# Kernel optimization log

Measured on AMD Instinct MI355X. Metric: run time of the kernel, lower is better.

## Reference

```python
import jax, jax.numpy as jnp
import numpy as np

D_MODEL = 512
N_HEADS = 8
D_K = D_MODEL // N_HEADS


def setup_inputs() -> dict:
    key = jax.random.key(0)
    ks = jax.random.split(key, 11)
    B, S = 4, 2048
    scale = 1.0 / np.sqrt(D_MODEL)
    inp = {
        'q': jax.random.normal(ks[0], (B, S, D_MODEL), jnp.float32),
        'k': jax.random.normal(ks[1], (B, S, D_MODEL), jnp.float32),
        'v': jax.random.normal(ks[2], (B, S, D_MODEL), jnp.float32),
        'wq': jax.random.normal(ks[3], (D_MODEL, D_MODEL), jnp.float32) * scale,
        'wk': jax.random.normal(ks[4], (D_MODEL, D_MODEL), jnp.float32) * scale,
        'wv': jax.random.normal(ks[5], (D_MODEL, D_MODEL), jnp.float32) * scale,
        'wo': jax.random.normal(ks[6], (D_MODEL, D_MODEL), jnp.float32) * scale,
        'bq': jax.random.normal(ks[7], (D_MODEL,), jnp.float32) * 0.01,
        'bk': jax.random.normal(ks[8], (D_MODEL,), jnp.float32) * 0.01,
        'bv': jax.random.normal(ks[9], (D_MODEL,), jnp.float32) * 0.01,
        'bo': jax.random.normal(ks[10], (D_MODEL,), jnp.float32) * 0.01,
    }
    return inp


def reference(q, k, v, wq, wk, wv, wo, bq, bk, bv, bo):
    b, s, d = q.shape
    # projections; torch Linear is x @ W.T + b
    qh = (q @ wq.T + bq).reshape(b, s, N_HEADS, D_K).transpose(0, 2, 1, 3)  # [b,h,s,dk]
    kh = (k @ wk.T + bk).reshape(b, s, N_HEADS, D_K).transpose(0, 2, 1, 3)
    vh = (v @ wv.T + bv).reshape(b, s, N_HEADS, D_K).transpose(0, 2, 1, 3)
    att = jnp.einsum('bhqd,bhkd->bhqk', qh, kh) / jnp.sqrt(jnp.float32(D_K))
    att = jax.nn.softmax(att, axis=-1)
    out = jnp.einsum('bhqk,bhkd->bhqd', att, vh)  # [b,h,s,dk]
    out = out.transpose(0, 2, 1, 3).reshape(b, s, d)
    return out @ wo.T + bo
```

## Files before the change

kernel.cpp:

```cpp
#include <hip/hip_runtime.h>

#define D_MODEL 512
#define NH 8
#define DK 64
#define SEQ 2048
#define NB 4

typedef __bf16 bf16x8 __attribute__((ext_vector_type(8)));
typedef float floatx4 __attribute__((ext_vector_type(4)));
typedef float floatx16 __attribute__((ext_vector_type(16)));

typedef __attribute__((address_space(1))) const unsigned int glb_u32;
typedef __attribute__((address_space(3))) unsigned int lds_u32;

__device__ __forceinline__ void gload_lds16(const unsigned short* g, unsigned short* l) {
    __builtin_amdgcn_global_load_lds((glb_u32*)g, (lds_u32*)l, 16, 0, 0);
}

__device__ inline unsigned int pack2bf(float lo, float hi) {
    unsigned int a = __float_as_uint(lo) + 0x8000u;
    unsigned int b = __float_as_uint(hi) + 0x8000u;
    return __builtin_amdgcn_perm(b, a, 0x07060302u);
}
__device__ inline unsigned short f2bf(float f) {
    return (unsigned short)((__float_as_uint(f) + 0x8000u) >> 16);
}
__device__ inline unsigned int scale2bf(unsigned int u, float s) {
    float lo = __uint_as_float(u << 16) * s;
    float hi = __uint_as_float(u & 0xFFFF0000u) * s;
    return pack2bf(lo, hi);
}

__global__ __launch_bounds__(256) void convert_kernel(
    const float* __restrict__ q, const float* __restrict__ k, const float* __restrict__ v,
    const float* __restrict__ wq, const float* __restrict__ wk, const float* __restrict__ wv,
    const float* __restrict__ wo, unsigned short* __restrict__ Xbf,
    unsigned short* __restrict__ Wbf)
{
    const int bid = blockIdx.x;
    const float* src;
    unsigned short* dst;
    size_t off;
    if (bid < 6144) {
        const int which = bid >> 11;
        src = (which == 0) ? q : (which == 1) ? k : v;
        dst = Xbf + (size_t)which * 4194304;
        off = ((size_t)(bid & 2047) * 256 + threadIdx.x) * 8;
    } else {
        const int wb = bid - 6144;
        const int which = wb >> 7;
        src = (which == 0) ? wq : (which == 1) ? wk : (which == 2) ? wv : wo;
        dst = Wbf + (size_t)which * 262144;
        off = ((size_t)(wb & 127) * 256 + threadIdx.x) * 8;
    }
    float4 a = *(const float4*)(src + off);
    float4 b = *(const float4*)(src + off + 4);
    uint4 r;
    r.x = pack2bf(a.x, a.y); r.y = pack2bf(a.z, a.w);
    r.z = pack2bf(b.x, b.y); r.w = pack2bf(b.z, b.w);
    *(uint4*)(dst + off) = r;
}

__global__ __launch_bounds__(256) void proj_qkv_kernel(
    const unsigned short* __restrict__ Xbf, const unsigned short* __restrict__ Wbf,
    const float* __restrict__ bq, const float* __restrict__ bk, const float* __restrict__ bv,
    unsigned short* __restrict__ Qh, unsigned short* __restrict__ Kh,
    unsigned short* __restrict__ VhT)
{
    const int which = blockIdx.z;
    const unsigned short* A = Xbf + (size_t)which * 4194304;
    const unsigned short* B = Wbf + (size_t)which * 262144;
    const float* bias = (which == 0) ? bq : (which == 1) ? bk : bv;

    const int n0 = blockIdx.x * 128;
    const int m0 = blockIdx.y * 128;

    __shared__ unsigned short lds[17408];

    const int tid  = threadIdx.x;
    const int lane = tid & 63;
    const int wid  = tid >> 6;
    const int quad = lane >> 4;
    const int l16  = lane & 15;
    const int wr   = (wid >> 1) * 64;
    const int wc   = (wid & 1) * 64;

    const int srow8 = lane >> 3;
    const int scg   = (lane & 7) ^ (srow8 & 7);

    floatx4 acc[4][4];
#pragma unroll
    for (int i = 0; i < 4; ++i)
#pragma unroll
        for (int j = 0; j < 4; ++j) acc[i][j] = {0.f, 0.f, 0.f, 0.f};

    for (int kt = 0; kt < 8; ++kt) {
        const int kk0 = kt * 64;
        __syncthreads();
#pragma unroll
        for (int t = 0; t < 4; ++t) {
            const int i = wid * 4 + t;
            const int row = i * 8 + srow8;
            gload_lds16(A + (size_t)(m0 + row) * 512 + kk0 + scg * 8, &lds[i * 512]);
            gload_lds16(B + (size_t)(n0 + row) * 512 + kk0 + scg * 8, &lds[8192 + i * 512]);
        }
        __syncthreads();

        bf16x8 af[4][2], bf[4][2];
#pragma unroll
        for (int kk = 0; kk < 2; ++kk) {
            const int c = kk * 4 + quad;
#pragma unroll
            for (int mi = 0; mi < 4; ++mi) {
                const int rA = wr + mi * 16 + l16;
                af[mi][kk] = *(const bf16x8*)(&lds[rA * 64 + ((c ^ (rA & 7)) * 8)]);
            }
#pragma unroll
            for (int ni = 0; ni < 4; ++ni) {
                const int rB = wc + ni * 16 + l16;
                bf[ni][kk] = *(const bf16x8*)(&lds[8192 + rB * 64 + ((c ^ (rB & 7)) * 8)]);
            }
        }
#pragma unroll
        for (int kk = 0; kk < 2; ++kk)
#pragma unroll
            for (int mi = 0; mi < 4; ++mi)
#pragma unroll
                for (int ni = 0; ni < 4; ++ni)
                    acc[mi][ni] = __builtin_amdgcn_mfma_f32_16x16x32_bf16(
                        af[mi][kk], bf[ni][kk], acc[mi][ni], 0, 0, 0);
    }

    float bs[4];
#pragma unroll
    for (int ni = 0; ni < 4; ++ni) bs[ni] = bias[n0 + wc + ni * 16 + l16];

    __syncthreads();
#pragma unroll
    for (int mi = 0; mi < 4; ++mi)
#pragma unroll
        for (int ni = 0; ni < 4; ++ni)
#pragma unroll
            for (int r = 0; r < 4; ++r)
                lds[(wr + mi * 16 + quad * 4 + r) * 136 + wc + ni * 16 + l16] =
                    f2bf(acc[mi][ni][r] + bs[ni]);
    __syncthreads();

    const int b = m0 >> 11;
    if (which != 2) {
        unsigned short* dst = (which == 0) ? Qh : Kh;
#pragma unroll
        for (int j = 0; j < 8; ++j) {
            const int chunk = j * 256 + tid;
            const int srow  = chunk >> 4;
            const int col   = (chunk & 15) * 8;
            const int h  = (n0 + col) >> 6;
            const int dk = col & 63;
            const int s  = (m0 & 2047) + srow;
            uint4 vv = *(const uint4*)(&lds[srow * 136 + col]);
            *(uint4*)(dst + ((size_t)(b * NH + h) * SEQ + s) * DK + dk) = vv;
        }
    } else {
#pragma unroll
        for (int j = 0; j < 8; ++j) {
            const int chunk = j * 256 + tid;
            const int d    = chunk >> 4;
            const int sc8  = (chunk & 15) * 8;
            const int h  = (n0 + d) >> 6;
            const int dk = (n0 + d) & 63;
            unsigned short tmp[8];
#pragma unroll
            for (int i = 0; i < 8; ++i) tmp[i] = lds[(sc8 + i) * 136 + d];
            const size_t s0 = (size_t)(m0 & 2047) + sc8;
            *(uint4*)(VhT + ((size_t)(b * NH + h) * DK + dk) * SEQ + s0) = *(const uint4*)tmp;
        }
    }
}

__global__ __launch_bounds__(256, 2) void flash_kernel(
    const unsigned short* __restrict__ Qh, const unsigned short* __restrict__ Kh,
    const unsigned short* __restrict__ VhT, unsigned short* __restrict__ AO)
{
    const int qt = blockIdx.x, h = blockIdx.y, b = blockIdx.z;
    const size_t bh = (size_t)b * NH + h;
    const unsigned short* Qp = Qh + bh * SEQ * DK;
    const unsigned short* Kp = Kh + bh * SEQ * DK;
    const unsigned short* Vp = VhT + bh * DK * SEQ;

    __shared__ unsigned short smem[17920];

    const int tid  = threadIdx.x;
    const int lane = tid & 63;
    const int wid  = tid >> 6;
    const int g    = wid >> 1;
    const int ws   = wid & 1;
    const int hh   = lane >> 5;
    const int l32  = lane & 31;

    const int srow = lane >> 3;
    const int schk = (lane & 7) ^ srow;

    const float SC = 0.18033688f;
    bf16x8 qf[4][2];
#pragma unroll
    for (int nt = 0; nt < 2; ++nt) {
        const int qrow = qt * 128 + ws * 64 + nt * 32 + l32;
#pragma unroll
        for (int ks = 0; ks < 4; ++ks) {
            uint4 u = *(const uint4*)(Qp + (size_t)qrow * 64 + ks * 16 + hh * 8);
            union { uint4 u4; bf16x8 v; } w;
            w.u4.x = scale2bf(u.x, SC); w.u4.y = scale2bf(u.y, SC);
            w.u4.z = scale2bf(u.z, SC); w.u4.w = scale2bf(u.w, SC);
            qf[ks][nt] = w.v;
        }
    }

    floatx16 oacc[2][2];
#pragma unroll
    for (int i = 0; i < 2; ++i)
#pragma unroll
        for (int j = 0; j < 2; ++j)
#pragma unroll
            for (int r = 0; r < 16; ++r) oacc[i][j][r] = 0.f;
    float lsA[2] = {0.f, 0.f}, lsB[2] = {0.f, 0.f};

    for (int kt = 0; kt < 16; ++kt) {
        __syncthreads();
#pragma unroll
        for (int t = 0; t < 8; ++t) {
            const int id = wid * 8 + t;
            const int gg = id >> 4;
            const int kv = (id >> 3) & 1;
            const int j  = id & 7;
            const int row = j * 8 + srow;
            const int sk0 = (gg * 16 + kt) * 64;
            if (kv == 0)
                gload_lds16(Kp + (size_t)(sk0 + row) * 64 + schk * 8,
                            &smem[gg * 8192 + j * 512]);
            else
                gload_lds16(Vp + (size_t)row * 2048 + sk0 + schk * 8,
                            &smem[gg * 8192 + 4096 + j * 512]);
        }
        __syncthreads();

        const unsigned short* Kb = &smem[g * 8192];
        const unsigned short* Vb = &smem[g * 8192 + 4096];

        floatx16 sc[2][2];
#pragma unroll
        for (int i = 0; i < 2; ++i)
#pragma unroll
            for (int j = 0; j < 2; ++j)
#pragma unroll
                for (int r = 0; r < 16; ++r) sc[i][j][r] = 0.f;
#pragma unroll
        for (int ks = 0; ks < 4; ++ks) {
            const int c = ks * 2 + hh;
            bf16x8 kf[2];
#pragma unroll
            for (int mt = 0; mt < 2; ++mt) {
                const int row = mt * 32 + l32;
                kf[mt] = *(const bf16x8*)(&Kb[row * 64 + ((c ^ (row & 7)) * 8)]);
            }
#pragma unroll
            for (int mt = 0; mt < 2; ++mt)
#pragma unroll
                for (int nt = 0; nt < 2; ++nt)
                    sc[mt][nt] = __builtin_amdgcn_mfma_f32_32x32x16_bf16(
                        kf[mt], qf[ks][nt], sc[mt][nt], 0, 0, 0);
        }

#pragma unroll
        for (int st = 0; st < 2; ++st)
#pragma unroll
            for (int nt = 0; nt < 2; ++nt)
#pragma unroll
                for (int r = 0; r < 16; ++r) {
                    float p = __builtin_amdgcn_exp2f(sc[st][nt][r]);
                    sc[st][nt][r] = p;
                    if (r & 1) lsB[nt] += p; else lsA[nt] += p;
                }

        bf16x8 vf[2][4];
#pragma unroll
        for (int ksp = 0; ksp < 4; ++ksp) {
            const int c = ksp * 2 + hh;
#pragma unroll
            for (int vt = 0; vt < 2; ++vt) {
                const int row = vt * 32 + l32;
                vf[vt][ksp] = *(const bf16x8*)(&Vb[row * 64 + ((c ^ (row & 7)) * 8)]);
            }
        }

#pragma unroll
        for (int st = 0; st < 2; ++st)
#pragma unroll
            for (int nt = 0; nt < 2; ++nt) {
                int p[8];
#pragma unroll
                for (int i = 0; i < 8; ++i)
                    p[i] = (int)pack2bf(sc[st][nt][2 * i], sc[st][nt][2 * i + 1]);
                const int e0 = __shfl_xor(hh ? p[0] : p[2], 32, 64);
                const int e1 = __shfl_xor(hh ? p[1] : p[3], 32, 64);
                const int e2 = __shfl_xor(hh ? p[4] : p[6], 32, 64);
                const int e3 = __shfl_xor(hh ? p[5] : p[7], 32, 64);
                union { int i4[4]; bf16x8 v; } b0, b1;
                b0.i4[0] = hh ? e0 : p[0];
                b0.i4[1] = hh ? e1 : p[1];
                b0.i4[2] = hh ? p[2] : e0;
                b0.i4[3] = hh ? p[3] : e1;
                b1.i4[0] = hh ? e2 : p[4];
                b1.i4[1] = hh ? e3 : p[5];
                b1.i4[2] = hh ? p[6] : e2;
                b1.i4[3] = hh ? p[7] : e3;
                const int k0 = st * 2;
#pragma unroll
                for (int vt = 0; vt < 2; ++vt) {
                    oacc[vt][nt] = __builtin_amdgcn_mfma_f32_32x32x16_bf16(
                        vf[vt][k0], b0.v, oacc[vt][nt], 0, 0, 0);
                    oacc[vt][nt] = __builtin_amdgcn_mfma_f32_32x32x16_bf16(
                        vf[vt][k0 + 1], b1.v, oacc[vt][nt], 0, 0, 0);
                }
            }
    }

    __syncthreads();
    float* pf = (float*)smem;
    float* lf = (float*)(&smem[17408]);
    if (g == 1) {
#pragma unroll
        for (int vt = 0; vt < 2; ++vt)
#pragma unroll
            for (int nt = 0; nt < 2; ++nt) {
                const int base = ws * 4352 + lane * 68 + (vt * 2 + nt) * 16;
#pragma unroll
                for (int r4 = 0; r4 < 4; ++r4) {
                    floatx4 t = {oacc[vt][nt][r4 * 4 + 0], oacc[vt][nt][r4 * 4 + 1],
                                 oacc[vt][nt][r4 * 4 + 2], oacc[vt][nt][r4 * 4 + 3]};
                    *(floatx4*)(&pf[base + r4 * 4]) = t;
                }
            }
        lf[ws * 128 + 0 * 64 + lane] = lsA[0] + lsB[0];
        lf[ws * 128 + 1 * 64 + lane] = lsA[1] + lsB[1];
    }
    __syncthreads();
    float linv[2];
    if (g == 0) {
#pragma unroll
        for (int nt = 0; nt < 2; ++nt) {
            float lm = lsA[nt] + lsB[nt] + lf[ws * 128 + nt * 64 + lane];
            lm += __shfl_xor(lm, 32, 64);
            linv[nt] = 1.0f / lm;
        }
#pragma unroll
        for (int vt = 0; vt < 2; ++vt)
#pragma unroll
            for (int nt = 0; nt < 2; ++nt) {
                const int base = ws * 4352 + lane * 68 + (vt * 2 + nt) * 16;
#pragma unroll
                for (int r4 = 0; r4 < 4; ++r4) {
                    floatx4 t = *(const floatx4*)(&pf[base + r4 * 4]);
#pragma unroll
                    for (int e = 0; e < 4; ++e)
                        oacc[vt][nt][r4 * 4 + e] =
                            (oacc[vt][nt][r4 * 4 + e] + t[e]) * linv[nt];
                }
            }
    }
    __syncthreads();
    if (g == 0) {
#pragma unroll
        for (int vt = 0; vt < 2; ++vt)
#pragma unroll
            for (int nt = 0; nt < 2; ++nt) {
                const int qrow = ws * 64 + nt * 32 + l32;
#pragma unroll
                for (int i = 0; i < 8; ++i) {
                    const int dko = vt * 32 + 8 * (i >> 1) + 2 * (i & 1) + 4 * hh;
                    *(unsigned int*)(&smem[qrow * 72 + dko]) =
                        pack2bf(oacc[vt][nt][2 * i], oacc[vt][nt][2 * i + 1]);
                }
            }
    }
    __syncthreads();
#pragma unroll
    for (int i = 0; i < 4; ++i) {
        const int idx = i * 256 + tid;
        const int row = idx >> 3;
        const int c   = idx & 7;
        *(uint4*)(AO + ((size_t)b * SEQ + qt * 128 + row) * 512 + h * 64 + c * 8) =
            *(const uint4*)(&smem[row * 72 + c * 8]);
    }
}

__global__ __launch_bounds__(256) void outproj_kernel(
    const unsigned short* __restrict__ AO, const unsigned short* __restrict__ Wbf,
    const float* __restrict__ bo, float* __restrict__ out)
{
    const unsigned short* B = Wbf + (size_t)3 * 262144;
    const int n0 = blockIdx.x * 128;
    const int m0 = blockIdx.y * 64;

    __shared__ unsigned short lds[12288];

    const int tid  = threadIdx.x;
    const int lane = tid & 63;
    const int wid  = tid >> 6;
    const int quad = lane >> 4;
    const int l16  = lane & 15;
    const int wr   = (wid >> 1) * 32;
    const int wc   = (wid & 1) * 64;

    const int srow8 = lane >> 3;
    const int scg   = (lane & 7) ^ (srow8 & 7);

    floatx4 acc[2][4];
#pragma unroll
    for (int i = 0; i < 2; ++i)
#pragma unroll
        for (int j = 0; j < 4; ++j) acc[i][j] = {0.f, 0.f, 0.f, 0.f};

    for (int kt = 0; kt < 8; ++kt) {
        const int kk0 = kt * 64;
        __syncthreads();
#pragma unroll
        for (int t = 0; t < 2; ++t) {
            const int i = wid * 2 + t;
            const int row = i * 8 + srow8;
            gload_lds16(AO + (size_t)(m0 + row) * 512 + kk0 + scg * 8, &lds[i * 512]);
        }
#pragma unroll
        for (int t = 0; t < 4; ++t) {
            const int i = wid * 4 + t;
            const int row = i * 8 + srow8;
            gload_lds16(B + (size_t)(n0 + row) * 512 + kk0 + scg * 8, &lds[4096 + i * 512]);
        }
        __syncthreads();

        bf16x8 af[2][2], bf[4][2];
#pragma unroll
        for (int kk = 0; kk < 2; ++kk) {
            const int c = kk * 4 + quad;
#pragma unroll
            for (int mi = 0; mi < 2; ++mi) {
                const int rA = wr + mi * 16 + l16;
                af[mi][kk] = *(const bf16x8*)(&lds[rA * 64 + ((c ^ (rA & 7)) * 8)]);
            }
#pragma unroll
            for (int ni = 0; ni < 4; ++ni) {
                const int rB = wc + ni * 16 + l16;
                bf[ni][kk] = *(const bf16x8*)(&lds[4096 + rB * 64 + ((c ^ (rB & 7)) * 8)]);
            }
        }
#pragma unroll
        for (int kk = 0; kk < 2; ++kk)
#pragma unroll
            for (int mi = 0; mi < 2; ++mi)
#pragma unroll
                for (int ni = 0; ni < 4; ++ni)
                    acc[mi][ni] = __builtin_amdgcn_mfma_f32_16x16x32_bf16(
                        af[mi][kk], bf[ni][kk], acc[mi][ni], 0, 0, 0);
    }

#pragma unroll
    for (int mi = 0; mi < 2; ++mi)
#pragma unroll
        for (int ni = 0; ni < 4; ++ni) {
            const int n = n0 + wc + ni * 16 + l16;
            const float bsv = bo[n];
#pragma unroll
            for (int r = 0; r < 4; ++r) {
                const int m = m0 + wr + mi * 16 + quad * 4 + r;
                out[(size_t)m * 512 + n] = acc[mi][ni][r] + bsv;
            }
        }
}

extern "C" void kernel_launch(void* const* d_in, const int* in_sizes, int n_in,
                              void* d_out, int out_size, void* d_ws, size_t ws_size,
                              hipStream_t stream) {
    const float* q  = (const float*)d_in[0];
    const float* k  = (const float*)d_in[1];
    const float* v  = (const float*)d_in[2];
    const float* wq = (const float*)d_in[3];
    const float* wk = (const float*)d_in[4];
    const float* wv = (const float*)d_in[5];
    const float* wo = (const float*)d_in[6];
    const float* bq = (const float*)d_in[7];
    const float* bk = (const float*)d_in[8];
    const float* bv = (const float*)d_in[9];
    const float* bo = (const float*)d_in[10];

    const size_t headElems = (size_t)NB * NH * SEQ * DK;
    unsigned short* Qh  = (unsigned short*)d_ws;
    unsigned short* Kh  = Qh + headElems;
    unsigned short* VhT = Kh + headElems;
    unsigned short* AO  = VhT + headElems;
    unsigned short* Xbf = AO + headElems;
    unsigned short* Wbf = Xbf + 3 * headElems;
    float* out = (float*)d_out;

    convert_kernel<<<dim3(6656), 256, 0, stream>>>(q, k, v, wq, wk, wv, wo, Xbf, Wbf);
    proj_qkv_kernel<<<dim3(4, 64, 3), 256, 0, stream>>>(
        Xbf, Wbf, bq, bk, bv, Qh, Kh, VhT);
    flash_kernel<<<dim3(SEQ / 128, NH, NB), 256, 0, stream>>>(Qh, Kh, VhT, AO);
    outproj_kernel<<<dim3(4, 128), 256, 0, stream>>>(AO, Wbf, bo, out);
}
```

Before: 192.5 us.

## Halve flash query tile to 64 rows and raise occupancy to 4 blocks per CU

The flash attention kernel now handles 64 query rows per block instead of 128, so each wave holds one 32-row Q fragment and half the score and output accumulators. Launch bounds go to 4 blocks per CU, shared memory shrinks, and V fragments are loaded from LDS just before each PV MFMA rather than all up front. The grid doubles to 1024 blocks. This cuts register pressure and raises occupancy to better hide latency, but each block reloads the full K/V for fewer queries, doubling K/V global and LDS traffic per unit of work.

Result: slower. 201.3 us (+4.6%).

```diff
diff --git a/kernel.cpp b/kernel.cpp
--- a/kernel.cpp
+++ b/kernel.cpp
@@ -177,7 +177,7 @@
     }
 }
 
-__global__ __launch_bounds__(256, 2) void flash_kernel(
+__global__ __launch_bounds__(256, 4) void flash_kernel(
     const unsigned short* __restrict__ Qh, const unsigned short* __restrict__ Kh,
     const unsigned short* __restrict__ VhT, unsigned short* __restrict__ AO)
 {
@@ -187,7 +187,7 @@
     const unsigned short* Kp = Kh + bh * SEQ * DK;
     const unsigned short* Vp = VhT + bh * DK * SEQ;
 
-    __shared__ unsigned short smem[17920];
+    __shared__ unsigned short smem[16384];
 
     const int tid  = threadIdx.x;
     const int lane = tid & 63;
@@ -201,28 +201,25 @@
     const int schk = (lane & 7) ^ srow;
 
     const float SC = 0.18033688f;
-    bf16x8 qf[4][2];
-#pragma unroll
-    for (int nt = 0; nt < 2; ++nt) {
-        const int qrow = qt * 128 + ws * 64 + nt * 32 + l32;
+    bf16x8 qf[4];
+    {
+        const int qrow = qt * 64 + ws * 32 + l32;
 #pragma unroll
         for (int ks = 0; ks < 4; ++ks) {
             uint4 u = *(const uint4*)(Qp + (size_t)qrow * 64 + ks * 16 + hh * 8);
             union { uint4 u4; bf16x8 v; } w;
             w.u4.x = scale2bf(u.x, SC); w.u4.y = scale2bf(u.y, SC);
             w.u4.z = scale2bf(u.z, SC); w.u4.w = scale2bf(u.w, SC);
-            qf[ks][nt] = w.v;
-        }
-    }
-
-    floatx16 oacc[2][2];
+            qf[ks] = w.v;
+        }
+    }
+
+    floatx16 oacc[2];
 #pragma unroll
     for (int i = 0; i < 2; ++i)
 #pragma unroll
-        for (int j = 0; j < 2; ++j)
-#pragma unroll
-            for (int r = 0; r < 16; ++r) oacc[i][j][r] = 0.f;
-    float lsA[2] = {0.f, 0.f}, lsB[2] = {0.f, 0.f};
+        for (int r = 0; r < 16; ++r) oacc[i][r] = 0.f;
+    float lsA = 0.f, lsB = 0.f;
 
     for (int kt = 0; kt < 16; ++kt) {
         __syncthreads();
@@ -246,149 +243,116 @@
         const unsigned short* Kb = &smem[g * 8192];
         const unsigned short* Vb = &smem[g * 8192 + 4096];
 
-        floatx16 sc[2][2];
+        floatx16 sc[2];
 #pragma unroll
         for (int i = 0; i < 2; ++i)
 #pragma unroll
-            for (int j = 0; j < 2; ++j)
-#pragma unroll
-                for (int r = 0; r < 16; ++r) sc[i][j][r] = 0.f;
+            for (int r = 0; r < 16; ++r) sc[i][r] = 0.f;
 #pragma unroll
         for (int ks = 0; ks < 4; ++ks) {
             const int c = ks * 2 + hh;
-            bf16x8 kf[2];
 #pragma unroll
             for (int mt = 0; mt < 2; ++mt) {
                 const int row = mt * 32 + l32;
-                kf[mt] = *(const bf16x8*)(&Kb[row * 64 + ((c ^ (row & 7)) * 8)]);
-            }
-#pragma unroll
-            for (int mt = 0; mt < 2; ++mt)
-#pragma unroll
-                for (int nt = 0; nt < 2; ++nt)
-                    sc[mt][nt] = __builtin_amdgcn_mfma_f32_32x32x16_bf16(
-                        kf[mt], qf[ks][nt], sc[mt][nt], 0, 0, 0);
+                bf16x8 kf = *(const bf16x8*)(&Kb[row * 64 + ((c ^ (row & 7)) * 8)]);
+                sc[mt] = __builtin_amdgcn_mfma_f32_32x32x16_bf16(
+                    kf, qf[ks], sc[mt], 0, 0, 0);
+            }
         }
 
 #pragma unroll
         for (int st = 0; st < 2; ++st)
 #pragma unroll
-            for (int nt = 0; nt < 2; ++nt)
-#pragma unroll
-                for (int r = 0; r < 16; ++r) {
-                    float p = __builtin_amdgcn_exp2f(sc[st][nt][r]);
-                    sc[st][nt][r] = p;
-                    if (r & 1) lsB[nt] += p; else lsA[nt] += p;
-                }
-
-        bf16x8 vf[2][4];
-#pragma unroll
-        for (int ksp = 0; ksp < 4; ++ksp) {
-            const int c = ksp * 2 + hh;
+            for (int r = 0; r < 16; ++r) {
+                float p = __builtin_amdgcn_exp2f(sc[st][r]);
+                sc[st][r] = p;
+                if (r & 1) lsB += p; else lsA += p;
+            }
+
+#pragma unroll
+        for (int st = 0; st < 2; ++st) {
+            int p[8];
+#pragma unroll
+            for (int i = 0; i < 8; ++i)
+                p[i] = (int)pack2bf(sc[st][2 * i], sc[st][2 * i + 1]);
+            const int e0 = __shfl_xor(hh ? p[0] : p[2], 32, 64);
+            const int e1 = __shfl_xor(hh ? p[1] : p[3], 32, 64);
+            const int e2 = __shfl_xor(hh ? p[4] : p[6], 32, 64);
+            const int e3 = __shfl_xor(hh ? p[5] : p[7], 32, 64);
+            union { int i4[4]; bf16x8 v; } b0, b1;
+            b0.i4[0] = hh ? e0 : p[0];
+            b0.i4[1] = hh ? e1 : p[1];
+            b0.i4[2] = hh ? p[2] : e0;
+            b0.i4[3] = hh ? p[3] : e1;
+            b1.i4[0] = hh ? e2 : p[4];
+            b1.i4[1] = hh ? e3 : p[5];
+            b1.i4[2] = hh ? p[6] : e2;
+            b1.i4[3] = hh ? p[7] : e3;
 #pragma unroll
             for (int vt = 0; vt < 2; ++vt) {
                 const int row = vt * 32 + l32;
-                vf[vt][ksp] = *(const bf16x8*)(&Vb[row * 64 + ((c ^ (row & 7)) * 8)]);
-            }
-        }
-
-#pragma unroll
-        for (int st = 0; st < 2; ++st)
-#pragma unroll
-            for (int nt = 0; nt < 2; ++nt) {
-                int p[8];
-#pragma unroll
-                for (int i = 0; i < 8; ++i)
-                    p[i] = (int)pack2bf(sc[st][nt][2 * i], sc[st][nt][2 * i + 1]);
-                const int e0 = __shfl_xor(hh ? p[0] : p[2], 32, 64);
-                const int e1 = __shfl_xor(hh ? p[1] : p[3], 32, 64);
-                const int e2 = __shfl_xor(hh ? p[4] : p[6], 32, 64);
-                const int e3 = __shfl_xor(hh ? p[5] : p[7], 32, 64);
-                union { int i4[4]; bf16x8 v; } b0, b1;
-                b0.i4[0] = hh ? e0 : p[0];
-                b0.i4[1] = hh ? e1 : p[1];
-                b0.i4[2] = hh ? p[2] : e0;
-                b0.i4[3] = hh ? p[3] : e1;
-                b1.i4[0] = hh ? e2 : p[4];
-                b1.i4[1] = hh ? e3 : p[5];
-                b1.i4[2] = hh ? p[6] : e2;
-                b1.i4[3] = hh ? p[7] : e3;
-                const int k0 = st * 2;
-#pragma unroll
-                for (int vt = 0; vt < 2; ++vt) {
-                    oacc[vt][nt] = __builtin_amdgcn_mfma_f32_32x32x16_bf16(
-                        vf[vt][k0], b0.v, oacc[vt][nt], 0, 0, 0);
-                    oacc[vt][nt] = __builtin_amdgcn_mfma_f32_32x32x16_bf16(
-                        vf[vt][k0 + 1], b1.v, oacc[vt][nt], 0, 0, 0);
-                }
-            }
+                const int c0 = (st * 2) * 2 + hh;
+                const int c1 = (st * 2 + 1) * 2 + hh;
+                bf16x8 vf0 = *(const bf16x8*)(&Vb[row * 64 + ((c0 ^ (row & 7)) * 8)]);
+                bf16x8 vf1 = *(const bf16x8*)(&Vb[row * 64 + ((c1 ^ (row & 7)) * 8)]);
+                oacc[vt] = __builtin_amdgcn_mfma_f32_32x32x16_bf16(
+                    vf0, b0.v, oacc[vt], 0, 0, 0);
+                oacc[vt] = __builtin_amdgcn_mfma_f32_32x32x16_bf16(
+                    vf1, b1.v, oacc[vt], 0, 0, 0);
+            }
+        }
     }
 
     __syncthreads();
     float* pf = (float*)smem;
-    float* lf = (float*)(&smem[17408]);
+    float* lf = (float*)(&smem[8704]);
     if (g == 1) {
+        const int base = (ws * 64 + lane) * 34;
 #pragma unroll
         for (int vt = 0; vt < 2; ++vt)
 #pragma unroll
-            for (int nt = 0; nt < 2; ++nt) {
-                const int base = ws * 4352 + lane * 68 + (vt * 2 + nt) * 16;
-#pragma unroll
-                for (int r4 = 0; r4 < 4; ++r4) {
-                    floatx4 t = {oacc[vt][nt][r4 * 4 + 0], oacc[vt][nt][r4 * 4 + 1],
-                                 oacc[vt][nt][r4 * 4 + 2], oacc[vt][nt][r4 * 4 + 3]};
-                    *(floatx4*)(&pf[base + r4 * 4]) = t;
-                }
-            }
-        lf[ws * 128 + 0 * 64 + lane] = lsA[0] + lsB[0];
-        lf[ws * 128 + 1 * 64 + lane] = lsA[1] + lsB[1];
-    }
-    __syncthreads();
-    float linv[2];
+            for (int r4 = 0; r4 < 4; ++r4) {
+                floatx4 t = {oacc[vt][r4 * 4 + 0], oacc[vt][r4 * 4 + 1],
+                             oacc[vt][r4 * 4 + 2], oacc[vt][r4 * 4 + 3]};
+                *(floatx4*)(&pf[base + vt * 16 + r4 * 4]) = t;
+            }
+        lf[ws * 64 + lane] = lsA + lsB;
+    }
+    __syncthreads();
     if (g == 0) {
-#pragma unroll
-        for (int nt = 0; nt < 2; ++nt) {
-            float lm = lsA[nt] + lsB[nt] + lf[ws * 128 + nt * 64 + lane];
-            lm += __shfl_xor(lm, 32, 64);
-            linv[nt] = 1.0f / lm;
-        }
+        float lm = lsA + lsB + lf[ws * 64 + lane];
+        lm += __shfl_xor(lm, 32, 64);
+        const float linv = 1.0f / lm;
+        const int base = (ws * 64 + lane) * 34;
 #pragma unroll
         for (int vt = 0; vt < 2; ++vt)
 #pragma unroll
-            for (int nt = 0; nt < 2; ++nt) {
-                const int base = ws * 4352 + lane * 68 + (vt * 2 + nt) * 16;
-#pragma unroll
-                for (int r4 = 0; r4 < 4; ++r4) {
-                    floatx4 t = *(const floatx4*)(&pf[base + r4 * 4]);
-#pragma unroll
-                    for (int e = 0; e < 4; ++e)
-                        oacc[vt][nt][r4 * 4 + e] =
-                            (oacc[vt][nt][r4 * 4 + e] + t[e]) * linv[nt];
-                }
+            for (int r4 = 0; r4 < 4; ++r4) {
+                floatx4 t = *(const floatx4*)(&pf[base + vt * 16 + r4 * 4]);
+#pragma unroll
+                for (int e = 0; e < 4; ++e)
+                    oacc[vt][r4 * 4 + e] = (oacc[vt][r4 * 4 + e] + t[e]) * linv;
             }
     }
     __syncthreads();
     if (g == 0) {
+        const int qrowl = ws * 32 + l32;
 #pragma unroll
         for (int vt = 0; vt < 2; ++vt)
 #pragma unroll
-            for (int nt = 0; nt < 2; ++nt) {
-                const int qrow = ws * 64 + nt * 32 + l32;
-#pragma unroll
-                for (int i = 0; i < 8; ++i) {
-                    const int dko = vt * 32 + 8 * (i >> 1) + 2 * (i & 1) + 4 * hh;
-                    *(unsigned int*)(&smem[qrow * 72 + dko]) =
-                        pack2bf(oacc[vt][nt][2 * i], oacc[vt][nt][2 * i + 1]);
-                }
-            }
-    }
-    __syncthreads();
-#pragma unroll
-    for (int i = 0; i < 4; ++i) {
+            for (int i = 0; i < 8; ++i) {
+                const int dko = vt * 32 + 8 * (i >> 1) + 2 * (i & 1) + 4 * hh;
+                *(unsigned int*)(&smem[qrowl * 72 + dko]) =
+                    pack2bf(oacc[vt][2 * i], oacc[vt][2 * i + 1]);
+            }
+    }
+    __syncthreads();
+#pragma unroll
+    for (int i = 0; i < 2; ++i) {
         const int idx = i * 256 + tid;
         const int row = idx >> 3;
         const int c   = idx & 7;
-        *(uint4*)(AO + ((size_t)b * SEQ + qt * 128 + row) * 512 + h * 64 + c * 8) =
+        *(uint4*)(AO + ((size_t)b * SEQ + qt * 64 + row) * 512 + h * 64 + c * 8) =
             *(const uint4*)(&smem[row * 72 + c * 8]);
     }
 }
@@ -503,6 +467,6 @@
     convert_kernel<<<dim3(6656), 256, 0, stream>>>(q, k, v, wq, wk, wv, wo, Xbf, Wbf);
     proj_qkv_kernel<<<dim3(4, 64, 3), 256, 0, stream>>>(
         Xbf, Wbf, bq, bk, bv, Qh, Kh, VhT);
-    flash_kernel<<<dim3(SEQ / 128, NH, NB), 256, 0, stream>>>(Qh, Kh, VhT, AO);
+    flash_kernel<<<dim3(32, NH, NB), 256, 0, stream>>>(Qh, Kh, VhT, AO);
     outproj_kernel<<<dim3(4, 128), 256, 0, stream>>>(AO, Wbf, bo, out);
 }
```

## Fuse fp32-to-bf16 conversion into projections and double-buffer flash K/V tiles

Applied to the files above, without the earlier changes.

Drops the separate conversion kernel. The QKV and output projections now read fp32 inputs and weights directly and convert them to bf16 while staging into padded LDS. This removes one launch and a bf16 write-and-reread of the inputs, but the projection loads are now synchronous register loads rather than async global-to-LDS loads, and the QKV K-tile is halved. The flash kernel adds double-buffered K/V staging with a changed swizzle so the next tile loads while the current one computes, which doubles its LDS use and may lower occupancy.

After: 216.3 us. +12.4%, slower.

```diff
diff --git a/kernel.cpp b/kernel.cpp
--- a/kernel.cpp
+++ b/kernel.cpp
@@ -31,45 +31,16 @@
     return pack2bf(lo, hi);
 }
 
-__global__ __launch_bounds__(256) void convert_kernel(
+__global__ __launch_bounds__(256) void proj_qkv_kernel(
     const float* __restrict__ q, const float* __restrict__ k, const float* __restrict__ v,
     const float* __restrict__ wq, const float* __restrict__ wk, const float* __restrict__ wv,
-    const float* __restrict__ wo, unsigned short* __restrict__ Xbf,
-    unsigned short* __restrict__ Wbf)
-{
-    const int bid = blockIdx.x;
-    const float* src;
-    unsigned short* dst;
-    size_t off;
-    if (bid < 6144) {
-        const int which = bid >> 11;
-        src = (which == 0) ? q : (which == 1) ? k : v;
-        dst = Xbf + (size_t)which * 4194304;
-        off = ((size_t)(bid & 2047) * 256 + threadIdx.x) * 8;
-    } else {
-        const int wb = bid - 6144;
-        const int which = wb >> 7;
-        src = (which == 0) ? wq : (which == 1) ? wk : (which == 2) ? wv : wo;
-        dst = Wbf + (size_t)which * 262144;
-        off = ((size_t)(wb & 127) * 256 + threadIdx.x) * 8;
-    }
-    float4 a = *(const float4*)(src + off);
-    float4 b = *(const float4*)(src + off + 4);
-    uint4 r;
-    r.x = pack2bf(a.x, a.y); r.y = pack2bf(a.z, a.w);
-    r.z = pack2bf(b.x, b.y); r.w = pack2bf(b.z, b.w);
-    *(uint4*)(dst + off) = r;
-}
-
-__global__ __launch_bounds__(256) void proj_qkv_kernel(
-    const unsigned short* __restrict__ Xbf, const unsigned short* __restrict__ Wbf,
     const float* __restrict__ bq, const float* __restrict__ bk, const float* __restrict__ bv,
     unsigned short* __restrict__ Qh, unsigned short* __restrict__ Kh,
     unsigned short* __restrict__ VhT)
 {
     const int which = blockIdx.z;
-    const unsigned short* A = Xbf + (size_t)which * 4194304;
-    const unsigned short* B = Wbf + (size_t)which * 262144;
+    const float* X    = (which == 0) ? q  : (which == 1) ? k  : v;
+    const float* W    = (which == 0) ? wq : (which == 1) ? wk : wv;
     const float* bias = (which == 0) ? bq : (which == 1) ? bk : bv;
 
     const int n0 = blockIdx.x * 128;
@@ -85,50 +56,42 @@
     const int wr   = (wid >> 1) * 64;
     const int wc   = (wid & 1) * 64;
 
-    const int srow8 = lane >> 3;
-    const int scg   = (lane & 7) ^ (srow8 & 7);
-
     floatx4 acc[4][4];
 #pragma unroll
     for (int i = 0; i < 4; ++i)
 #pragma unroll
         for (int j = 0; j < 4; ++j) acc[i][j] = {0.f, 0.f, 0.f, 0.f};
 
-    for (int kt = 0; kt < 8; ++kt) {
-        const int kk0 = kt * 64;
+    for (int kt = 0; kt < 16; ++kt) {
+        const int kk0 = kt * 32;
         __syncthreads();
 #pragma unroll
-        for (int t = 0; t < 4; ++t) {
-            const int i = wid * 4 + t;
-            const int row = i * 8 + srow8;
-            gload_lds16(A + (size_t)(m0 + row) * 512 + kk0 + scg * 8, &lds[i * 512]);
-            gload_lds16(B + (size_t)(n0 + row) * 512 + kk0 + scg * 8, &lds[8192 + i * 512]);
+        for (int i = 0; i < 4; ++i) {
+            int f   = tid + i * 256;
+            int row = f >> 3;
+            int kq  = (f & 7) * 4;
+            float4 a4 = *(const float4*)(X + (size_t)(m0 + row) * 512 + kk0 + kq);
+            uint2 ap2; ap2.x = pack2bf(a4.x, a4.y); ap2.y = pack2bf(a4.z, a4.w);
+            *(uint2*)(&lds[row * 40 + kq]) = ap2;
+            float4 b4 = *(const float4*)(W + (size_t)(n0 + row) * 512 + kk0 + kq);
+            uint2 bp2; bp2.x = pack2bf(b4.x, b4.y); bp2.y = pack2bf(b4.z, b4.w);
+            *(uint2*)(&lds[5120 + row * 40 + kq]) = bp2;
         }
         __syncthreads();
 
-        bf16x8 af[4][2], bf[4][2];
-#pragma unroll
-        for (int kk = 0; kk < 2; ++kk) {
-            const int c = kk * 4 + quad;
-#pragma unroll
-            for (int mi = 0; mi < 4; ++mi) {
-                const int rA = wr + mi * 16 + l16;
-                af[mi][kk] = *(const bf16x8*)(&lds[rA * 64 + ((c ^ (rA & 7)) * 8)]);
-            }
-#pragma unroll
-            for (int ni = 0; ni < 4; ++ni) {
-                const int rB = wc + ni * 16 + l16;
-                bf[ni][kk] = *(const bf16x8*)(&lds[8192 + rB * 64 + ((c ^ (rB & 7)) * 8)]);
-            }
-        }
-#pragma unroll
-        for (int kk = 0; kk < 2; ++kk)
-#pragma unroll
-            for (int mi = 0; mi < 4; ++mi)
-#pragma unroll
-                for (int ni = 0; ni < 4; ++ni)
-                    acc[mi][ni] = __builtin_amdgcn_mfma_f32_16x16x32_bf16(
-                        af[mi][kk], bf[ni][kk], acc[mi][ni], 0, 0, 0);
+        bf16x8 af[4], bfr[4];
+#pragma unroll
+        for (int mi = 0; mi < 4; ++mi)
+            af[mi] = *(const bf16x8*)(&lds[(wr + mi * 16 + l16) * 40 + quad * 8]);
+#pragma unroll
+        for (int ni = 0; ni < 4; ++ni)
+            bfr[ni] = *(const bf16x8*)(&lds[5120 + (wc + ni * 16 + l16) * 40 + quad * 8]);
+#pragma unroll
+        for (int mi = 0; mi < 4; ++mi)
+#pragma unroll
+            for (int ni = 0; ni < 4; ++ni)
+                acc[mi][ni] = __builtin_amdgcn_mfma_f32_16x16x32_bf16(
+                    af[mi], bfr[ni], acc[mi][ni], 0, 0, 0);
     }
 
     float bs[4];
@@ -187,7 +150,7 @@
     const unsigned short* Kp = Kh + bh * SEQ * DK;
     const unsigned short* Vp = VhT + bh * DK * SEQ;
 
-    __shared__ unsigned short smem[17920];
+    __shared__ unsigned short smem[32768];
 
     const int tid  = threadIdx.x;
     const int lane = tid & 63;
@@ -196,9 +159,7 @@
     const int ws   = wid & 1;
     const int hh   = lane >> 5;
     const int l32  = lane & 31;
-
     const int srow = lane >> 3;
-    const int schk = (lane & 7) ^ srow;
 
     const float SC = 0.18033688f;
     bf16x8 qf[4][2];
@@ -224,8 +185,7 @@
             for (int r = 0; r < 16; ++r) oacc[i][j][r] = 0.f;
     float lsA[2] = {0.f, 0.f}, lsB[2] = {0.f, 0.f};
 
-    for (int kt = 0; kt < 16; ++kt) {
-        __syncthreads();
+    auto stage = [&](int d, int kt) {
 #pragma unroll
         for (int t = 0; t < 8; ++t) {
             const int id = wid * 8 + t;
@@ -233,18 +193,25 @@
             const int kv = (id >> 3) & 1;
             const int j  = id & 7;
             const int row = j * 8 + srow;
+            const int sg  = (lane & 7) ^ srow ^ j;
             const int sk0 = (gg * 16 + kt) * 64;
+            unsigned short* dstl = &smem[d * 16384 + gg * 8192 + kv * 4096 + j * 512];
             if (kv == 0)
-                gload_lds16(Kp + (size_t)(sk0 + row) * 64 + schk * 8,
-                            &smem[gg * 8192 + j * 512]);
+                gload_lds16(Kp + (size_t)(sk0 + row) * 64 + sg * 8, dstl);
             else
-                gload_lds16(Vp + (size_t)row * 2048 + sk0 + schk * 8,
-                            &smem[gg * 8192 + 4096 + j * 512]);
-        }
+                gload_lds16(Vp + (size_t)row * 2048 + sk0 + sg * 8, dstl);
+        }
+    };
+
+    stage(0, 0);
+
+    for (int kt = 0; kt < 16; ++kt) {
         __syncthreads();
-
-        const unsigned short* Kb = &smem[g * 8192];
-        const unsigned short* Vb = &smem[g * 8192 + 4096];
+        if (kt < 15) stage((kt + 1) & 1, kt + 1);
+
+        const int d = kt & 1;
+        const unsigned short* Kb = &smem[d * 16384 + g * 8192];
+        const unsigned short* Vb = &smem[d * 16384 + g * 8192 + 4096];
 
         floatx16 sc[2][2];
 #pragma unroll
@@ -260,7 +227,8 @@
 #pragma unroll
             for (int mt = 0; mt < 2; ++mt) {
                 const int row = mt * 32 + l32;
-                kf[mt] = *(const bf16x8*)(&Kb[row * 64 + ((c ^ (row & 7)) * 8)]);
+                const int ch  = (c ^ (row & 7) ^ ((row >> 3) & 7)) * 8;
+                kf[mt] = *(const bf16x8*)(&Kb[row * 64 + ch]);
             }
 #pragma unroll
             for (int mt = 0; mt < 2; ++mt)
@@ -288,7 +256,8 @@
 #pragma unroll
             for (int vt = 0; vt < 2; ++vt) {
                 const int row = vt * 32 + l32;
-                vf[vt][ksp] = *(const bf16x8*)(&Vb[row * 64 + ((c ^ (row & 7)) * 8)]);
+                const int ch  = (c ^ (row & 7) ^ ((row >> 3) & 7)) * 8;
+                vf[vt][ksp] = *(const bf16x8*)(&Vb[row * 64 + ch]);
             }
         }
 
@@ -344,8 +313,8 @@
         lf[ws * 128 + 1 * 64 + lane] = lsA[1] + lsB[1];
     }
     __syncthreads();
-    float linv[2];
     if (g == 0) {
+        float linv[2];
 #pragma unroll
         for (int nt = 0; nt < 2; ++nt) {
             float lm = lsA[nt] + lsB[nt] + lf[ws * 128 + nt * 64 + lane];
@@ -394,14 +363,13 @@
 }
 
 __global__ __launch_bounds__(256) void outproj_kernel(
-    const unsigned short* __restrict__ AO, const unsigned short* __restrict__ Wbf,
+    const unsigned short* __restrict__ AO, const float* __restrict__ wo,
     const float* __restrict__ bo, float* __restrict__ out)
 {
-    const unsigned short* B = Wbf + (size_t)3 * 262144;
     const int n0 = blockIdx.x * 128;
     const int m0 = blockIdx.y * 64;
 
-    __shared__ unsigned short lds[12288];
+    __shared__ unsigned short lds[13312];
 
     const int tid  = threadIdx.x;
     const int lane = tid & 63;
@@ -412,7 +380,7 @@
     const int wc   = (wid & 1) * 64;
 
     const int srow8 = lane >> 3;
-    const int scg   = (lane & 7) ^ (srow8 & 7);
+    const int scg   = (lane & 7) ^ srow8;
 
     floatx4 acc[2][4];
 #pragma unroll
@@ -430,14 +398,17 @@
             gload_lds16(AO + (size_t)(m0 + row) * 512 + kk0 + scg * 8, &lds[i * 512]);
         }
 #pragma unroll
-        for (int t = 0; t < 4; ++t) {
-            const int i = wid * 4 + t;
-            const int row = i * 8 + srow8;
-            gload_lds16(B + (size_t)(n0 + row) * 512 + kk0 + scg * 8, &lds[4096 + i * 512]);
+        for (int i = 0; i < 8; ++i) {
+            int f   = tid + i * 256;
+            int row = f >> 4;
+            int col = (f & 15) * 4;
+            float4 b4 = *(const float4*)(wo + (size_t)(n0 + row) * 512 + kk0 + col);
+            uint2 bp2; bp2.x = pack2bf(b4.x, b4.y); bp2.y = pack2bf(b4.z, b4.w);
+            *(uint2*)(&lds[4096 + row * 72 + col]) = bp2;
         }
         __syncthreads();
 
-        bf16x8 af[2][2], bf[4][2];
+        bf16x8 af[2][2], bfr[4][2];
 #pragma unroll
         for (int kk = 0; kk < 2; ++kk) {
             const int c = kk * 4 + quad;
@@ -449,7 +420,7 @@
 #pragma unroll
             for (int ni = 0; ni < 4; ++ni) {
                 const int rB = wc + ni * 16 + l16;
-                bf[ni][kk] = *(const bf16x8*)(&lds[4096 + rB * 64 + ((c ^ (rB & 7)) * 8)]);
+                bfr[ni][kk] = *(const bf16x8*)(&lds[4096 + rB * 72 + c * 8]);
             }
         }
 #pragma unroll
@@ -459,7 +430,7 @@
 #pragma unroll
                 for (int ni = 0; ni < 4; ++ni)
                     acc[mi][ni] = __builtin_amdgcn_mfma_f32_16x16x32_bf16(
-                        af[mi][kk], bf[ni][kk], acc[mi][ni], 0, 0, 0);
+                        af[mi][kk], bfr[ni][kk], acc[mi][ni], 0, 0, 0);
     }
 
 #pragma unroll
@@ -496,13 +467,10 @@
     unsigned short* Kh  = Qh + headElems;
     unsigned short* VhT = Kh + headElems;
     unsigned short* AO  = VhT + headElems;
-    unsigned short* Xbf = AO + headElems;
-    unsigned short* Wbf = Xbf + 3 * headElems;
     float* out = (float*)d_out;
 
-    convert_kernel<<<dim3(6656), 256, 0, stream>>>(q, k, v, wq, wk, wv, wo, Xbf, Wbf);
     proj_qkv_kernel<<<dim3(4, 64, 3), 256, 0, stream>>>(
-        Xbf, Wbf, bq, bk, bv, Qh, Kh, VhT);
+        q, k, v, wq, wk, wv, bq, bk, bv, Qh, Kh, VhT);
     flash_kernel<<<dim3(SEQ / 128, NH, NB), 256, 0, stream>>>(Qh, Kh, VhT, AO);
-    outproj_kernel<<<dim3(4, 128), 256, 0, stream>>>(AO, Wbf, bo, out);
-}
+    outproj_kernel<<<dim3(4, 128), 256, 0, stream>>>(AO, wo, bo, out);
+}
```
